# Performance work log

Measured on AMD Instinct MI355X. Metric: run time of the kernel, lower is better.

## Reference

```python
import jax, jax.numpy as jnp
import numpy as np

N_NODES = 100000
IN_CH = 128
HID = 128   # 2 * out_channels
OUT = 64
N_EDGES = 1600000


def gcn_conv(x, W, b, src, dst, n_nodes):
    """PyG GCNConv: add self-loops, symmetric normalization D^-1/2 (A+I) D^-1/2 X W + b."""
    h = x @ W  # [N, F_out]
    ones = jnp.ones(dst.shape[0], dtype=h.dtype)
    # degree of target nodes, +1 for self loop
    deg = jax.ops.segment_sum(ones, dst, num_segments=n_nodes) + 1.0
    dinv = jnp.where(deg > 0, jax.lax.rsqrt(deg), 0.0)  # [N]
    norm = dinv[src] * dinv[dst]  # [E]
    agg = jax.ops.segment_sum(h[src] * norm[:, None], dst, num_segments=n_nodes)
    # self-loop contribution: norm_ii = dinv_i^2 (avoids materializing extra edges)
    agg = agg + h * (dinv * dinv)[:, None]
    return agg + b


def setup_inputs() -> dict:
    key = jax.random.key(0)
    ks = jax.random.split(key, 8)
    x = jax.random.normal(ks[0], (N_NODES, IN_CH), dtype=jnp.float32)
    edge_index = jax.random.randint(ks[1], (2, N_EDGES), 0, N_NODES, dtype=jnp.int64)
    # Glorot-style params
    W1 = jax.random.normal(ks[2], (IN_CH, HID), dtype=jnp.float32) / np.sqrt(IN_CH)
    b1 = jnp.zeros((HID,), dtype=jnp.float32)
    W_mu = jax.random.normal(ks[3], (HID, OUT), dtype=jnp.float32) / np.sqrt(HID)
    b_mu = jnp.zeros((OUT,), dtype=jnp.float32)
    W_ls = jax.random.normal(ks[4], (HID, OUT), dtype=jnp.float32) / np.sqrt(HID)
    b_ls = jnp.zeros((OUT,), dtype=jnp.float32)
    return {"x": x, "edge_index": edge_index, "W1": W1, "b1": b1,
            "W_mu": W_mu, "b_mu": b_mu, "W_ls": W_ls, "b_ls": b_ls}


def reference(x, edge_index, W1, b1, W_mu, b_mu, W_ls, b_ls):
    src, dst = edge_index[0], edge_index[1]
    n = x.shape[0]
    h = jax.nn.relu(gcn_conv(x, W1, b1, src, dst, n))
    mu = gcn_conv(h, W_mu, b_mu, src, dst, n)
    logstd = gcn_conv(h, W_ls, b_ls, src, dst, n)
    return (mu, logstd)
```

## Files before the change

### kernel.cpp

```cpp
#include <hip/hip_runtime.h>
#include <hip/hip_bf16.h>
#include <stdint.h>

#define N_NODES 100000
#define IN_CH   128
#define HID     128
#define OUT_CH  64
#define N_EDGES 1600000

#define NB    196
#define NBLK  250
#define EPB   6400

typedef __attribute__((ext_vector_type(8))) short  bf16x8;
typedef __attribute__((ext_vector_type(4))) float  f32x4;


__device__ __forceinline__ unsigned short f2bf(float f) {
    unsigned int u = __float_as_uint(f);
    u = (u + 0x7fffu + ((u >> 16) & 1u)) >> 16;
    return (unsigned short)u;
}
__device__ __forceinline__ float bfl(unsigned int u) { return __uint_as_float(u << 16); }
__device__ __forceinline__ float bfh(unsigned int u) { return __uint_as_float(u & 0xffff0000u); }


__global__ __launch_bounds__(256) void k_phaseA(const int* __restrict__ dst,
                                                int* __restrict__ Cm) {
    __shared__ int hist[NB];
    int blk = blockIdx.x, t = threadIdx.x;
    if (t < NB) hist[t] = 0;
    __syncthreads();
    int base = blk * EPB;
#pragma unroll 5
    for (int k = 0; k < EPB / 256; k++) {
        int d = dst[base + k * 256 + t];
        atomicAdd(&hist[d >> 9], 1);
    }
    __syncthreads();
    if (t < NB) Cm[blk * NB + t] = hist[t];
}

__global__ __launch_bounds__(256) void k_scanBkt(int* __restrict__ Cm,
                                                 int* __restrict__ bktSum) {
    __shared__ int sdata[256];
    int b = blockIdx.x, t = threadIdx.x;
    int v = (t < NBLK) ? Cm[t * NB + b] : 0;
    sdata[t] = v;
    __syncthreads();
    int val = v;
    for (int off = 1; off < 256; off <<= 1) {
        int tmp = (t >= off) ? sdata[t - off] : 0;
        __syncthreads();
        val += tmp;
        sdata[t] = val;
        __syncthreads();
    }
    if (t < NBLK) Cm[t * NB + b] = val - v;
    if (t == 255) bktSum[b] = val;
}

__global__ __launch_bounds__(256) void k_scanBase(const int* __restrict__ bktSum,
                                                  int* __restrict__ bktBase) {
    __shared__ int sdata[256];
    int t = threadIdx.x;
    int v = (t < NB) ? bktSum[t] : 0;
    sdata[t] = v;
    __syncthreads();
    int val = v;
    for (int off = 1; off < 256; off <<= 1) {
        int tmp = (t >= off) ? sdata[t - off] : 0;
        __syncthreads();
        val += tmp;
        sdata[t] = val;
        __syncthreads();
    }
    if (t < NB) bktBase[t] = val - v;
    if (t == 0) bktBase[NB] = N_EDGES;
}

__global__ __launch_bounds__(256) void k_phaseB(const int* __restrict__ src,
                                                const int* __restrict__ dst,
                                                const int* __restrict__ Cm,
                                                const int* __restrict__ bktBase,
                                                unsigned int* __restrict__ bucketed) {
    __shared__ int offs[NB];
    int blk = blockIdx.x, t = threadIdx.x;
    if (t < NB) offs[t] = Cm[blk * NB + t] + bktBase[t];
    __syncthreads();
    int base = blk * EPB;
#pragma unroll 5
    for (int k = 0; k < EPB / 256; k++) {
        int e = base + k * 256 + t;
        int d = dst[e];
        int sv = src[e];
        int pos = atomicAdd(&offs[d >> 9], 1);
        bucketed[pos] = ((unsigned int)sv << 9) | (unsigned int)(d & 511);
    }
}

__global__ __launch_bounds__(512) void k_phaseC(const unsigned int* __restrict__ bucketed,
                                                const int* __restrict__ bktBase,
                                                int* __restrict__ rowptr,
                                                float* __restrict__ dinvg,
                                                int* __restrict__ csr_src) {
    __shared__ int cnt[512];
    __shared__ int cur[512];
    __shared__ int sdata[512];
    int b = blockIdx.x, t = threadIdx.x;
    int base = bktBase[b], endR = bktBase[b + 1];
    int nodeBase = b << 9;
    int nNodes = N_NODES - nodeBase;
    if (nNodes > 512) nNodes = 512;

    cnt[t] = 0;
    __syncthreads();
    for (int e = base + t; e < endR; e += 512)
        atomicAdd(&cnt[bucketed[e] & 511], 1);
    __syncthreads();

    int s = cnt[t];
    sdata[t] = s;
    __syncthreads();
    int val = s;
    for (int off = 1; off < 512; off <<= 1) {
        int tmp = (t >= off) ? sdata[t - off] : 0;
        __syncthreads();
        val += tmp;
        sdata[t] = val;
        __syncthreads();
    }
    cur[t] = val - s;
    if (t < nNodes) {
        rowptr[nodeBase + t] = base + val - s;
        dinvg[nodeBase + t] = rsqrtf((float)s + 1.0f);
    }
    if (b == NB - 1 && t == 0) rowptr[N_NODES] = N_EDGES;
    __syncthreads();

    for (int e = base + t; e < endR; e += 512) {
        unsigned int u = bucketed[e];
        int pos = base + atomicAdd(&cur[u & 511], 1);
        csr_src[pos] = (int)(u >> 9);
    }
}


__global__ __launch_bounds__(256) void k_prepW(const float* __restrict__ W1,
                                               const float* __restrict__ Wmu,
                                               const float* __restrict__ Wls,
                                               unsigned short* __restrict__ Wt1,
                                               unsigned short* __restrict__ WtC) {
    int idx = blockIdx.x * 256 + threadIdx.x;
    int n = idx >> 7, k = idx & 127;
    Wt1[idx] = f2bf(W1[k * 128 + n]);
    WtC[idx] = f2bf((n < 64) ? Wmu[k * 64 + n] : Wls[k * 64 + (n - 64)]);
}


#define LDA 136

__global__ __launch_bounds__(256) void k_gemm1(const float* __restrict__ X,
                                               const unsigned short* __restrict__ Wt,
                                               unsigned short* __restrict__ Y) {
    __shared__ unsigned short sA[128 * LDA];
    int t = threadIdx.x;
    int R0 = blockIdx.x * 128;
    int row = t >> 1, colb = (t & 1) * 64;
    bool valid = (R0 + row) < N_NODES;
    const float* Xr = X + (size_t)(R0 + row) * 128 + colb;
    unsigned short* dp = sA + row * LDA + colb;
#pragma unroll
    for (int j = 0; j < 16; j++) {
        float4 v = valid ? *(const float4*)(Xr + j * 4) : make_float4(0.f, 0.f, 0.f, 0.f);
        ushort4 o;
        o.x = f2bf(v.x); o.y = f2bf(v.y); o.z = f2bf(v.z); o.w = f2bf(v.w);
        *(ushort4*)(dp + j * 4) = o;
    }
    __syncthreads();

    int wv = t >> 6, l = t & 63;
    int quad = l >> 4, lm = l & 15;

    bf16x8 a[2][4];
#pragma unroll
    for (int mt = 0; mt < 2; mt++)
#pragma unroll
        for (int ks = 0; ks < 4; ks++)
            a[mt][ks] = *(const bf16x8*)(sA + (wv * 32 + mt * 16 + lm) * LDA +
                                         ks * 32 + quad * 8);

    f32x4 acc[2][8] = {};
#pragma unroll
    for (int nt = 0; nt < 8; nt++) {
        bf16x8 b[4];
        const unsigned short* Wp = Wt + (nt * 16 + lm) * 128 + quad * 8;
#pragma unroll
        for (int ks = 0; ks < 4; ks++)
            b[ks] = *(const bf16x8*)(Wp + ks * 32);
#pragma unroll
        for (int mt = 0; mt < 2; mt++) {
            f32x4 c = acc[mt][nt];
#pragma unroll
            for (int ks = 0; ks < 4; ks++)
                c = __builtin_amdgcn_mfma_f32_16x16x32_bf16(a[mt][ks], b[ks], c, 0, 0, 0);
            acc[mt][nt] = c;
        }
    }

    int rbase = R0 + wv * 32 + quad * 4;
#pragma unroll
    for (int mt = 0; mt < 2; mt++)
#pragma unroll
        for (int nt = 0; nt < 8; nt++)
#pragma unroll
            for (int reg = 0; reg < 4; reg++) {
                int r = rbase + mt * 16 + reg;
                if (r < N_NODES)
                    Y[(size_t)r * 128 + nt * 16 + lm] = f2bf(acc[mt][nt][reg]);
            }
}


__global__ __launch_bounds__(256) void k_agg1(const unsigned short* __restrict__ h0,
                                              const int* __restrict__ rowptr,
                                              const int* __restrict__ csr_src,
                                              const float* __restrict__ dinv,
                                              const float* __restrict__ b1,
                                              unsigned short* __restrict__ hb) {
    int lane = threadIdx.x & 63;
    int i = __builtin_amdgcn_readfirstlane(blockIdx.x * 4 + (threadIdx.x >> 6));
    int c2 = lane * 2;
    float di = dinv[i];
    unsigned int sv = *(const unsigned int*)(h0 + (size_t)i * 128 + c2);
    float ax = bfl(sv) * di * di, ay = bfh(sv) * di * di;
    int beg = rowptr[i], end = rowptr[i + 1];
    for (int p = beg; p < end; p += 16) {
        int s[16]; float n[16]; unsigned int r[16];
#pragma unroll
        for (int j = 0; j < 16; j++) {
            int q = p + j;
            s[j] = csr_src[q < end ? q : end - 1];
        }
#pragma unroll
        for (int j = 0; j < 16; j++) n[j] = dinv[s[j]];
#pragma unroll
        for (int j = 0; j < 16; j++)
            r[j] = *(const unsigned int*)(h0 + (size_t)s[j] * 128 + c2);
#pragma unroll
        for (int j = 0; j < 16; j++) n[j] = (p + j < end) ? n[j] * di : 0.f;
#pragma unroll
        for (int j = 0; j < 16; j++) {
            ax = fmaf(bfl(r[j]), n[j], ax);
            ay = fmaf(bfh(r[j]), n[j], ay);
        }
    }
    ax += b1[c2];
    ay += b1[c2 + 1];
    ax = ax > 0.f ? ax : 0.f;
    ay = ay > 0.f ? ay : 0.f;
    unsigned int pk = ((unsigned int)f2bf(ay) << 16) | (unsigned int)f2bf(ax);
    *(unsigned int*)(hb + (size_t)i * 128 + c2) = pk;
}


#define LDG 136

__global__ __launch_bounds__(256) void k_agg2g(const unsigned short* __restrict__ hb,
                                               const int* __restrict__ rowptr,
                                               const int* __restrict__ csr_src,
                                               const float* __restrict__ dinv,
                                               const unsigned short* __restrict__ WtC,
                                               const float* __restrict__ bmu,
                                               const float* __restrict__ bls,
                                               float* __restrict__ out) {
    __shared__ unsigned short g[16 * LDG];
    int t = threadIdx.x;
    int wv = t >> 6, lane = t & 63;
    int nodeBase = blockIdx.x * 16;
    int c2 = lane * 2;

#pragma unroll 1
    for (int j4 = 0; j4 < 4; j4++) {
        int i = __builtin_amdgcn_readfirstlane(nodeBase + wv * 4 + j4);
        float di = dinv[i];
        unsigned int sv = *(const unsigned int*)(hb + (size_t)i * 128 + c2);
        float ax = bfl(sv) * di * di, ay = bfh(sv) * di * di;
        int beg = rowptr[i], end = rowptr[i + 1];
        for (int p = beg; p < end; p += 16) {
            int s[16]; float n[16]; unsigned int r[16];
#pragma unroll
            for (int j = 0; j < 16; j++) {
                int q = p + j;
                s[j] = csr_src[q < end ? q : end - 1];
            }
#pragma unroll
            for (int j = 0; j < 16; j++) n[j] = dinv[s[j]];
#pragma unroll
            for (int j = 0; j < 16; j++)
                r[j] = *(const unsigned int*)(hb + (size_t)s[j] * 128 + c2);
#pragma unroll
            for (int j = 0; j < 16; j++) n[j] = (p + j < end) ? n[j] * di : 0.f;
#pragma unroll
            for (int j = 0; j < 16; j++) {
                ax = fmaf(bfl(r[j]), n[j], ax);
                ay = fmaf(bfh(r[j]), n[j], ay);
            }
        }
        unsigned int pk = ((unsigned int)f2bf(ay) << 16) | (unsigned int)f2bf(ax);
        *(unsigned int*)(g + (wv * 4 + j4) * LDG + c2) = pk;
    }
    __syncthreads();

    int quad = lane >> 4, lm = lane & 15;
    bf16x8 a[4];
#pragma unroll
    for (int ks = 0; ks < 4; ks++)
        a[ks] = *(const bf16x8*)(g + lm * LDG + ks * 32 + quad * 8);

#pragma unroll
    for (int nt2 = 0; nt2 < 2; nt2++) {
        int nt = wv * 2 + nt2;
        f32x4 acc = {};
        const unsigned short* Wp = WtC + (nt * 16 + lm) * 128 + quad * 8;
#pragma unroll
        for (int ks = 0; ks < 4; ks++) {
            bf16x8 b = *(const bf16x8*)(Wp + ks * 32);
            acc = __builtin_amdgcn_mfma_f32_16x16x32_bf16(a[ks], b, acc, 0, 0, 0);
        }
        int col = nt * 16 + lm;
#pragma unroll
        for (int reg = 0; reg < 4; reg++) {
            int row = nodeBase + quad * 4 + reg;
            float v = acc[reg];
            if (col < 64)
                out[(size_t)row * 64 + col] = v + bmu[col];
            else
                out[(size_t)N_NODES * 64 + (size_t)row * 64 + (col - 64)] = v + bls[col - 64];
        }
    }
}


extern "C" void kernel_launch(void* const* d_in, const int* in_sizes, int n_in,
                              void* d_out, int out_size, void* d_ws, size_t ws_size,
                              hipStream_t stream) {
    const float* x    = (const float*)d_in[0];
    const int*   ei   = (const int*)d_in[1];
    const float* W1   = (const float*)d_in[2];
    const float* b1   = (const float*)d_in[3];
    const float* Wmu  = (const float*)d_in[4];
    const float* bmu  = (const float*)d_in[5];
    const float* Wls  = (const float*)d_in[6];
    const float* bls  = (const float*)d_in[7];
    const int* src = ei;
    const int* dst = ei + N_EDGES;

    char* p = (char*)d_ws;
    unsigned short* bufA = (unsigned short*)p; p += (size_t)N_NODES * 128 * 2;
    unsigned short* bufH = (unsigned short*)p; p += (size_t)N_NODES * 128 * 2;
    unsigned short* Wt1  = (unsigned short*)p; p += 128 * 128 * 2;
    unsigned short* WtC  = (unsigned short*)p; p += 128 * 128 * 2;
    int*   Cm      = (int*)p;   p += (size_t)NBLK * NB * 4;
    int*   bktSum  = (int*)p;   p += 256 * 4;
    int*   bktBase = (int*)p;   p += 256 * 4;
    int*   rowptr  = (int*)p;   p += 400016;
    float* dinv    = (float*)p; p += 400000;
    unsigned int* bucketed = (unsigned int*)p; p += (size_t)N_EDGES * 4;
    int*   csr_src = (int*)p;   p += (size_t)N_EDGES * 4;

    k_phaseA<<<NBLK, 256, 0, stream>>>(dst, Cm);
    k_scanBkt<<<NB, 256, 0, stream>>>(Cm, bktSum);
    k_scanBase<<<1, 256, 0, stream>>>(bktSum, bktBase);
    k_phaseB<<<NBLK, 256, 0, stream>>>(src, dst, Cm, bktBase, bucketed);
    k_phaseC<<<NB, 512, 0, stream>>>(bucketed, bktBase, rowptr, dinv, csr_src);

    k_prepW<<<64, 256, 0, stream>>>(W1, Wmu, Wls, Wt1, WtC);

    int gblk = (N_NODES + 127) / 128;

    k_gemm1<<<gblk, 256, 0, stream>>>(x, Wt1, bufA);
    k_agg1<<<N_NODES / 4, 256, 0, stream>>>(bufA, rowptr, csr_src, dinv, b1, bufH);

    k_agg2g<<<N_NODES / 16, 256, 0, stream>>>(bufH, rowptr, csr_src, dinv,
                                              WtC, bmu, bls, (float*)d_out);
}
```

Baseline: 343.2 us.

## Switch intermediates to fp16 with half2 gather and 16-byte edge loads

Switches intermediate storage and the MFMA instructions from bf16 to fp16, and accumulates the neighbour gather with packed half2 FMAs. Each wavefront now splits into four groups of 16 lanes; each group handles a different edge with 16-byte row loads, and the partial sums are combined with cross-lane shuffles. The second aggregation now uses 4 nodes per block, so its MFMA tile is padded with 12 zero rows, and only the first quad writes results. This cuts load instructions and ALU work per edge. In exchange, fp16 accumulation loses precision and can overflow, and most of the second layer's matrix work is wasted on padding.

```diff
diff --git a/kernel.cpp b/kernel.cpp
--- a/kernel.cpp
+++ b/kernel.cpp
@@ -1,5 +1,6 @@
 #include <hip/hip_runtime.h>
 #include <hip/hip_bf16.h>
+#include <hip/hip_fp16.h>
 #include <stdint.h>
 
 #define N_NODES 100000
@@ -12,17 +13,10 @@
 #define NBLK  250
 #define EPB   6400
 
-typedef __attribute__((ext_vector_type(8))) short  bf16x8;
+typedef __attribute__((ext_vector_type(8))) short  s16x8;
 typedef __attribute__((ext_vector_type(4))) float  f32x4;
 
-
-__device__ __forceinline__ unsigned short f2bf(float f) {
-    unsigned int u = __float_as_uint(f);
-    u = (u + 0x7fffu + ((u >> 16) & 1u)) >> 16;
-    return (unsigned short)u;
-}
-__device__ __forceinline__ float bfl(unsigned int u) { return __uint_as_float(u << 16); }
-__device__ __forceinline__ float bfh(unsigned int u) { return __uint_as_float(u & 0xffff0000u); }
+union U4 { uint4 u; __half2 h[4]; unsigned int w[4]; };
 
 
 __global__ __launch_bounds__(256) void k_phaseA(const int* __restrict__ dst,
@@ -153,8 +147,10 @@
                                                unsigned short* __restrict__ WtC) {
     int idx = blockIdx.x * 256 + threadIdx.x;
     int n = idx >> 7, k = idx & 127;
-    Wt1[idx] = f2bf(W1[k * 128 + n]);
-    WtC[idx] = f2bf((n < 64) ? Wmu[k * 64 + n] : Wls[k * 64 + (n - 64)]);
+    __half a = __float2half(W1[k * 128 + n]);
+    __half b = __float2half((n < 64) ? Wmu[k * 64 + n] : Wls[k * 64 + (n - 64)]);
+    Wt1[idx] = *(unsigned short*)&a;
+    WtC[idx] = *(unsigned short*)&b;
 }
 
 
@@ -173,37 +169,40 @@
 #pragma unroll
     for (int j = 0; j < 16; j++) {
         float4 v = valid ? *(const float4*)(Xr + j * 4) : make_float4(0.f, 0.f, 0.f, 0.f);
-        ushort4 o;
-        o.x = f2bf(v.x); o.y = f2bf(v.y); o.z = f2bf(v.z); o.w = f2bf(v.w);
-        *(ushort4*)(dp + j * 4) = o;
+        __half2 p0 = __floats2half2_rn(v.x, v.y);
+        __half2 p1 = __floats2half2_rn(v.z, v.w);
+        uint2 o;
+        o.x = *(unsigned int*)&p0;
+        o.y = *(unsigned int*)&p1;
+        *(uint2*)(dp + j * 4) = o;
     }
     __syncthreads();
 
     int wv = t >> 6, l = t & 63;
     int quad = l >> 4, lm = l & 15;
 
-    bf16x8 a[2][4];
+    s16x8 a[2][4];
 #pragma unroll
     for (int mt = 0; mt < 2; mt++)
 #pragma unroll
         for (int ks = 0; ks < 4; ks++)
-            a[mt][ks] = *(const bf16x8*)(sA + (wv * 32 + mt * 16 + lm) * LDA +
-                                         ks * 32 + quad * 8);
+            a[mt][ks] = *(const s16x8*)(sA + (wv * 32 + mt * 16 + lm) * LDA +
+                                        ks * 32 + quad * 8);
 
     f32x4 acc[2][8] = {};
 #pragma unroll
     for (int nt = 0; nt < 8; nt++) {
-        bf16x8 b[4];
+        s16x8 b[4];
         const unsigned short* Wp = Wt + (nt * 16 + lm) * 128 + quad * 8;
 #pragma unroll
         for (int ks = 0; ks < 4; ks++)
-            b[ks] = *(const bf16x8*)(Wp + ks * 32);
+            b[ks] = *(const s16x8*)(Wp + ks * 32);
 #pragma unroll
         for (int mt = 0; mt < 2; mt++) {
             f32x4 c = acc[mt][nt];
 #pragma unroll
             for (int ks = 0; ks < 4; ks++)
-                c = __builtin_amdgcn_mfma_f32_16x16x32_bf16(a[mt][ks], b[ks], c, 0, 0, 0);
+                c = __builtin_amdgcn_mfma_f32_16x16x32_f16(a[mt][ks], b[ks], c, 0, 0, 0);
             acc[mt][nt] = c;
         }
     }
@@ -216,11 +215,69 @@
 #pragma unroll
             for (int reg = 0; reg < 4; reg++) {
                 int r = rbase + mt * 16 + reg;
-                if (r < N_NODES)
-                    Y[(size_t)r * 128 + nt * 16 + lm] = f2bf(acc[mt][nt][reg]);
+                if (r < N_NODES) {
+                    __half hv = __float2half(acc[mt][nt][reg]);
+                    Y[(size_t)r * 128 + nt * 16 + lm] = *(unsigned short*)&hv;
+                }
             }
 }
 
+
+#define AGG_GATHER(tbl)                                                        \
+    int l = threadIdx.x & 63;                                                  \
+    int wv = threadIdx.x >> 6;                                                 \
+    int i = __builtin_amdgcn_readfirstlane(blockIdx.x * 4 + wv);               \
+    int g = l >> 4, lm = l & 15;                                               \
+    float di = dinv[i];                                                        \
+    U4 rs; rs.u = *(const uint4*)((tbl) + (size_t)i * 128 + lm * 8);           \
+    float ns = (g == 0) ? di * di : 0.f;                                       \
+    __half2 ns2 = __floats2half2_rn(ns, ns);                                   \
+    __half2 acc0 = __hmul2(rs.h[0], ns2);                                      \
+    __half2 acc1 = __hmul2(rs.h[1], ns2);                                      \
+    __half2 acc2 = __hmul2(rs.h[2], ns2);                                      \
+    __half2 acc3 = __hmul2(rs.h[3], ns2);                                      \
+    int beg = rowptr[i], end = rowptr[i + 1];                                  \
+    for (int p = beg; p < end; p += 16) {                                      \
+        int s[4]; float n[4]; U4 r[4];                                         \
+        _Pragma("unroll")                                                      \
+        for (int j = 0; j < 4; j++) {                                          \
+            int q = p + j * 4 + g;                                             \
+            s[j] = csr_src[q < end ? q : end - 1];                             \
+        }                                                                      \
+        _Pragma("unroll")                                                      \
+        for (int j = 0; j < 4; j++) n[j] = dinv[s[j]];                         \
+        _Pragma("unroll")                                                      \
+        for (int j = 0; j < 4; j++)                                            \
+            r[j].u = *(const uint4*)((tbl) + (size_t)s[j] * 128 + lm * 8);     \
+        _Pragma("unroll")                                                      \
+        for (int j = 0; j < 4; j++) {                                          \
+            float nn = (p + j * 4 + g < end) ? n[j] * di : 0.f;                \
+            __half2 nh = __floats2half2_rn(nn, nn);                            \
+            acc0 = __hfma2(r[j].h[0], nh, acc0);                               \
+            acc1 = __hfma2(r[j].h[1], nh, acc1);                               \
+            acc2 = __hfma2(r[j].h[2], nh, acc2);                               \
+            acc3 = __hfma2(r[j].h[3], nh, acc3);                               \
+        }                                                                      \
+    }                                                                          \
+                                       \
+    {                                                                          \
+        int v0 = *(int*)&acc0, v1 = *(int*)&acc1,                              \
+            v2 = *(int*)&acc2, v3 = *(int*)&acc3;                              \
+        int u0 = __shfl_xor(v0, 16), u1 = __shfl_xor(v1, 16),                  \
+            u2 = __shfl_xor(v2, 16), u3 = __shfl_xor(v3, 16);                  \
+        acc0 = __hadd2(acc0, *(__half2*)&u0);                                  \
+        acc1 = __hadd2(acc1, *(__half2*)&u1);                                  \
+        acc2 = __hadd2(acc2, *(__half2*)&u2);                                  \
+        acc3 = __hadd2(acc3, *(__half2*)&u3);                                  \
+        v0 = *(int*)&acc0; v1 = *(int*)&acc1;                                  \
+        v2 = *(int*)&acc2; v3 = *(int*)&acc3;                                  \
+        u0 = __shfl_xor(v0, 32); u1 = __shfl_xor(v1, 32);                      \
+        u2 = __shfl_xor(v2, 32); u3 = __shfl_xor(v3, 32);                      \
+        acc0 = __hadd2(acc0, *(__half2*)&u0);                                  \
+        acc1 = __hadd2(acc1, *(__half2*)&u1);                                  \
+        acc2 = __hadd2(acc2, *(__half2*)&u2);                                  \
+        acc3 = __hadd2(acc3, *(__half2*)&u3);                                  \
+    }
 
 __global__ __launch_bounds__(256) void k_agg1(const unsigned short* __restrict__ h0,
                                               const int* __restrict__ rowptr,
@@ -228,39 +285,28 @@
                                               const float* __restrict__ dinv,
                                               const float* __restrict__ b1,
                                               unsigned short* __restrict__ hb) {
-    int lane = threadIdx.x & 63;
-    int i = __builtin_amdgcn_readfirstlane(blockIdx.x * 4 + (threadIdx.x >> 6));
-    int c2 = lane * 2;
-    float di = dinv[i];
-    unsigned int sv = *(const unsigned int*)(h0 + (size_t)i * 128 + c2);
-    float ax = bfl(sv) * di * di, ay = bfh(sv) * di * di;
-    int beg = rowptr[i], end = rowptr[i + 1];
-    for (int p = beg; p < end; p += 16) {
-        int s[16]; float n[16]; unsigned int r[16];
-#pragma unroll
-        for (int j = 0; j < 16; j++) {
-            int q = p + j;
-            s[j] = csr_src[q < end ? q : end - 1];
-        }
-#pragma unroll
-        for (int j = 0; j < 16; j++) n[j] = dinv[s[j]];
-#pragma unroll
-        for (int j = 0; j < 16; j++)
-            r[j] = *(const unsigned int*)(h0 + (size_t)s[j] * 128 + c2);
-#pragma unroll
-        for (int j = 0; j < 16; j++) n[j] = (p + j < end) ? n[j] * di : 0.f;
-#pragma unroll
-        for (int j = 0; j < 16; j++) {
-            ax = fmaf(bfl(r[j]), n[j], ax);
-            ay = fmaf(bfh(r[j]), n[j], ay);
-        }
-    }
-    ax += b1[c2];
-    ay += b1[c2 + 1];
-    ax = ax > 0.f ? ax : 0.f;
-    ay = ay > 0.f ? ay : 0.f;
-    unsigned int pk = ((unsigned int)f2bf(ay) << 16) | (unsigned int)f2bf(ax);
-    *(unsigned int*)(hb + (size_t)i * 128 + c2) = pk;
+    AGG_GATHER(h0)
+    if (l < 16) {
+        int cb = lm * 8;
+        float4 bA = *(const float4*)(b1 + cb);
+        float4 bB = *(const float4*)(b1 + cb + 4);
+        float2 f0 = __half22float2(acc0), f1 = __half22float2(acc1);
+        float2 f2 = __half22float2(acc2), f3 = __half22float2(acc3);
+        f0.x += bA.x; f0.y += bA.y; f1.x += bA.z; f1.y += bA.w;
+        f2.x += bB.x; f2.y += bB.y; f3.x += bB.z; f3.y += bB.w;
+        f0.x = f0.x > 0.f ? f0.x : 0.f;  f0.y = f0.y > 0.f ? f0.y : 0.f;
+        f1.x = f1.x > 0.f ? f1.x : 0.f;  f1.y = f1.y > 0.f ? f1.y : 0.f;
+        f2.x = f2.x > 0.f ? f2.x : 0.f;  f2.y = f2.y > 0.f ? f2.y : 0.f;
+        f3.x = f3.x > 0.f ? f3.x : 0.f;  f3.y = f3.y > 0.f ? f3.y : 0.f;
+        __half2 o0 = __floats2half2_rn(f0.x, f0.y);
+        __half2 o1 = __floats2half2_rn(f1.x, f1.y);
+        __half2 o2 = __floats2half2_rn(f2.x, f2.y);
+        __half2 o3 = __floats2half2_rn(f3.x, f3.y);
+        uint4 w;
+        w.x = *(unsigned int*)&o0; w.y = *(unsigned int*)&o1;
+        w.z = *(unsigned int*)&o2; w.w = *(unsigned int*)&o3;
+        *(uint4*)(hb + (size_t)i * 128 + cb) = w;
+    }
 }
 
 
@@ -274,50 +320,26 @@
                                                const float* __restrict__ bmu,
                                                const float* __restrict__ bls,
                                                float* __restrict__ out) {
-    __shared__ unsigned short g[16 * LDG];
-    int t = threadIdx.x;
-    int wv = t >> 6, lane = t & 63;
-    int nodeBase = blockIdx.x * 16;
-    int c2 = lane * 2;
-
-#pragma unroll 1
-    for (int j4 = 0; j4 < 4; j4++) {
-        int i = __builtin_amdgcn_readfirstlane(nodeBase + wv * 4 + j4);
-        float di = dinv[i];
-        unsigned int sv = *(const unsigned int*)(hb + (size_t)i * 128 + c2);
-        float ax = bfl(sv) * di * di, ay = bfh(sv) * di * di;
-        int beg = rowptr[i], end = rowptr[i + 1];
-        for (int p = beg; p < end; p += 16) {
-            int s[16]; float n[16]; unsigned int r[16];
-#pragma unroll
-            for (int j = 0; j < 16; j++) {
-                int q = p + j;
-                s[j] = csr_src[q < end ? q : end - 1];
-            }
-#pragma unroll
-            for (int j = 0; j < 16; j++) n[j] = dinv[s[j]];
-#pragma unroll
-            for (int j = 0; j < 16; j++)
-                r[j] = *(const unsigned int*)(hb + (size_t)s[j] * 128 + c2);
-#pragma unroll
-            for (int j = 0; j < 16; j++) n[j] = (p + j < end) ? n[j] * di : 0.f;
-#pragma unroll
-            for (int j = 0; j < 16; j++) {
-                ax = fmaf(bfl(r[j]), n[j], ax);
-                ay = fmaf(bfh(r[j]), n[j], ay);
-            }
-        }
-        unsigned int pk = ((unsigned int)f2bf(ay) << 16) | (unsigned int)f2bf(ax);
-        *(unsigned int*)(g + (wv * 4 + j4) * LDG + c2) = pk;
-    }
-    __syncthreads();
-
-    int quad = lane >> 4, lm = lane & 15;
-    bf16x8 a[4];
+    __shared__ unsigned short gls[16 * LDG];
+    {
+        for (int z = threadIdx.x; z < 12 * LDG; z += 256) gls[4 * LDG + z] = 0;
+    }
+    AGG_GATHER(hb)
+    if (l < 16) {
+        uint4 w;
+        w.x = *(unsigned int*)&acc0; w.y = *(unsigned int*)&acc1;
+        w.z = *(unsigned int*)&acc2; w.w = *(unsigned int*)&acc3;
+        *(uint4*)(gls + wv * LDG + lm * 8) = w;
+    }
+    __syncthreads();
+
+    int quad = l >> 4;
+    s16x8 a[4];
 #pragma unroll
     for (int ks = 0; ks < 4; ks++)
-        a[ks] = *(const bf16x8*)(g + lm * LDG + ks * 32 + quad * 8);
-
+        a[ks] = *(const s16x8*)(gls + lm * LDG + ks * 32 + quad * 8);
+
+    int nodeBase = blockIdx.x * 4;
 #pragma unroll
     for (int nt2 = 0; nt2 < 2; nt2++) {
         int nt = wv * 2 + nt2;
@@ -325,18 +347,21 @@
         const unsigned short* Wp = WtC + (nt * 16 + lm) * 128 + quad * 8;
 #pragma unroll
         for (int ks = 0; ks < 4; ks++) {
-            bf16x8 b = *(const bf16x8*)(Wp + ks * 32);
-            acc = __builtin_amdgcn_mfma_f32_16x16x32_bf16(a[ks], b, acc, 0, 0, 0);
+            s16x8 b = *(const s16x8*)(Wp + ks * 32);
+            acc = __builtin_amdgcn_mfma_f32_16x16x32_f16(a[ks], b, acc, 0, 0, 0);
         }
-        int col = nt * 16 + lm;
-#pragma unroll
-        for (int reg = 0; reg < 4; reg++) {
-            int row = nodeBase + quad * 4 + reg;
-            float v = acc[reg];
-            if (col < 64)
-                out[(size_t)row * 64 + col] = v + bmu[col];
-            else
-                out[(size_t)N_NODES * 64 + (size_t)row * 64 + (col - 64)] = v + bls[col - 64];
+        if (quad == 0) {
+            int col = nt * 16 + lm;
+#pragma unroll
+            for (int reg = 0; reg < 4; reg++) {
+                int row = nodeBase + reg;
+                float v = acc[reg];
+                if (col < 64)
+                    out[(size_t)row * 64 + col] = v + bmu[col];
+                else
+                    out[(size_t)N_NODES * 64 + (size_t)row * 64 + (col - 64)] =
+                        v + bls[col - 64];
+            }
         }
     }
 }
@@ -382,6 +407,6 @@
     k_gemm1<<<gblk, 256, 0, stream>>>(x, Wt1, bufA);
     k_agg1<<<N_NODES / 4, 256, 0, stream>>>(bufA, rowptr, csr_src, dinv, b1, bufH);
 
-    k_agg2g<<<N_NODES / 16, 256, 0, stream>>>(bufH, rowptr, csr_src, dinv,
-                                              WtC, bmu, bls, (float*)d_out);
-}
+    k_agg2g<<<N_NODES / 4, 256, 0, stream>>>(bufH, rowptr, csr_src, dinv,
+                                             WtC, bmu, bls, (float*)d_out);
+}
```

Measured after the change: 376.4 us. 9.7% more time.
